# Optimization experiments

Hardware: AMD Instinct MI355X
Metric: run time of the kernel (lower is better)

## Reference

```python
import jax, jax.numpy as jnp
import numpy as np

B, N, C, H, R = 4, 1568, 768, 12, 256
D = C // H
MLP_H = 4 * C
EPS = 1e-5  # torch LayerNorm default


def _ln(x, g, b):
    mu = jnp.mean(x, -1, keepdims=True)
    var = jnp.var(x, -1, keepdims=True)
    return (x - mu) / jnp.sqrt(var + EPS) * g + b


def setup_inputs() -> dict:
    key = jax.random.key(0)
    ks = jax.random.split(key, 6)
    s = 0.02
    return {
        "x": jax.random.normal(ks[0], (B, N, C), jnp.float32),
        "size": jnp.ones((B, N, 1), jnp.float32),  # ToMe token sizes
        "qkv_w": jax.random.normal(ks[1], (3 * C, C), jnp.float32) * s,
        "q_bias": jnp.zeros((C,), jnp.float32),
        "v_bias": jnp.zeros((C,), jnp.float32),
        "proj_w": jax.random.normal(ks[2], (C, C), jnp.float32) * s,
        "proj_b": jnp.zeros((C,), jnp.float32),
        "ln1_g": jnp.ones((C,), jnp.float32),
        "ln1_b": jnp.zeros((C,), jnp.float32),
        "ln2_g": jnp.ones((C,), jnp.float32),
        "ln2_b": jnp.zeros((C,), jnp.float32),
        "fc1_w": jax.random.normal(ks[3], (MLP_H, C), jnp.float32) * s,
        "fc1_b": jnp.zeros((MLP_H,), jnp.float32),
        "fc2_w": jax.random.normal(ks[4], (C, MLP_H), jnp.float32) * s,
        "fc2_b": jnp.zeros((C,), jnp.float32),
        "r": R,
    }


def reference(x, size, qkv_w, q_bias, v_bias, proj_w, proj_b,
              ln1_g, ln1_b, ln2_g, ln2_b, fc1_w, fc1_b, fc2_w, fc2_b, r):
    Bc, Nc, Cc = x.shape
    scale = D ** -0.5

    # ---- attention with log-size bias ----
    h = _ln(x, ln1_g, ln1_b)
    qkv_bias = jnp.concatenate([q_bias, jnp.zeros_like(v_bias), v_bias])
    qkv = h @ qkv_w.T + qkv_bias                      # [B,N,3C]
    qkv = qkv.reshape(Bc, Nc, 3, H, D).transpose(2, 0, 3, 1, 4)  # [3,B,H,N,D]
    q, k, v = qkv[0] * scale, qkv[1], qkv[2]
    attn = jnp.einsum('bhnd,bhmd->bhnm', q, k)
    attn = attn + jnp.log(size)[:, None, None, :, 0]  # per-key log-size bias
    attn = jax.nn.softmax(attn, axis=-1)
    o = jnp.einsum('bhnm,bhmd->bhnd', attn, v)
    o = o.transpose(0, 2, 1, 3).reshape(Bc, Nc, Cc)
    o = o @ proj_w.T + proj_b
    metric = k.mean(axis=1)                           # [B,N,D] mean over heads
    x = x + o

    # ---- bipartite soft matching (class_token=False, distill=False) ----
    m = metric / jnp.linalg.norm(metric, axis=-1, keepdims=True)
    a, bt = m[:, ::2], m[:, 1::2]                     # [B,Ta,D], [B,Tb,D]
    scores = jnp.einsum('bic,bjc->bij', a, bt)
    node_max = scores.max(axis=-1)                    # [B,Ta]
    node_idx = scores.argmax(axis=-1)                 # [B,Ta]
    edge_idx = jnp.argsort(-node_max, axis=-1)        # descending
    unm_idx = edge_idx[:, r:]                         # [B,Ta-r]
    src_idx = edge_idx[:, :r]                         # [B,r]
    dst_idx = jnp.take_along_axis(node_idx, src_idx, axis=-1)  # [B,r]

    def _merge_sum(t):  # t: [B,N,c]
        src, dst = t[:, ::2], t[:, 1::2]
        unm = jnp.take_along_axis(src, unm_idx[:, :, None], axis=1)
        sg = jnp.take_along_axis(src, src_idx[:, :, None], axis=1)
        dst = jax.vmap(lambda d, i, s: d.at[i].add(s))(dst, dst_idx, sg)
        return jnp.concatenate([unm, dst], axis=1)

    # merge_wavg: size-weighted average
    xm = _merge_sum(x * size)
    size_new = _merge_sum(size)
    x = xm / size_new                                 # [B,N-r,C]

    # ---- MLP ----
    h = _ln(x, ln2_g, ln2_b)
    h = jax.nn.gelu(h @ fc1_w.T + fc1_b, approximate=False)
    x = x + (h @ fc2_w.T + fc2_b)
    return x
```

## Files before the change

kernel.cpp:

```cpp
#include <hip/hip_runtime.h>
#include <stdint.h>

typedef unsigned short ushort_t;
typedef __attribute__((ext_vector_type(4))) float f32x4;
typedef __attribute__((ext_vector_type(8))) short bf16x8;

#define DEV __device__ __forceinline__

DEV ushort_t f2bf(float f) {
  uint32_t x = __float_as_uint(f);
  uint32_t r = (x + 0x7fffu + ((x >> 16) & 1u)) >> 16;
  return (ushort_t)r;
}

DEV f32x4 mfma16(bf16x8 a, bf16x8 b, f32x4 c) {
  return __builtin_amdgcn_mfma_f32_16x16x32_bf16(a, b, c, 0, 0, 0);
}

DEV bf16x8 ld_frag_lds(const ushort_t* p) {
  bf16x8 r;
  ((uint64_t*)&r)[0] = ((const uint64_t*)p)[0];
  ((uint64_t*)&r)[1] = ((const uint64_t*)p)[1];
  return r;
}
DEV bf16x8 ld_frag_g(const ushort_t* p) { return *(const bf16x8*)p; }

DEV float np_pw96(const float* a) {
  float r0 = a[0], r1 = a[1], r2 = a[2], r3 = a[3];
  float r4 = a[4], r5 = a[5], r6 = a[6], r7 = a[7];
  for (int i = 8; i < 96; i += 8) {
    r0 = __fadd_rn(r0, a[i]);     r1 = __fadd_rn(r1, a[i + 1]);
    r2 = __fadd_rn(r2, a[i + 2]); r3 = __fadd_rn(r3, a[i + 3]);
    r4 = __fadd_rn(r4, a[i + 4]); r5 = __fadd_rn(r5, a[i + 5]);
    r6 = __fadd_rn(r6, a[i + 6]); r7 = __fadd_rn(r7, a[i + 7]);
  }
  return __fadd_rn(__fadd_rn(__fadd_rn(r0, r1), __fadd_rn(r2, r3)),
                   __fadd_rn(__fadd_rn(r4, r5), __fadd_rn(r6, r7)));
}
DEV float np_pw768(const float* a) {
  float q0 = __fadd_rn(np_pw96(a +   0), np_pw96(a +  96));
  float q1 = __fadd_rn(np_pw96(a + 192), np_pw96(a + 288));
  float q2 = __fadd_rn(np_pw96(a + 384), np_pw96(a + 480));
  float q3 = __fadd_rn(np_pw96(a + 576), np_pw96(a + 672));
  return __fadd_rn(__fadd_rn(q0, q1), __fadd_rn(q2, q3));
}
DEV float np_pw64(const float* a) {
  float r0 = a[0], r1 = a[1], r2 = a[2], r3 = a[3];
  float r4 = a[4], r5 = a[5], r6 = a[6], r7 = a[7];
  for (int i = 8; i < 64; i += 8) {
    r0 = __fadd_rn(r0, a[i]);     r1 = __fadd_rn(r1, a[i + 1]);
    r2 = __fadd_rn(r2, a[i + 2]); r3 = __fadd_rn(r3, a[i + 3]);
    r4 = __fadd_rn(r4, a[i + 4]); r5 = __fadd_rn(r5, a[i + 5]);
    r6 = __fadd_rn(r6, a[i + 6]); r7 = __fadd_rn(r7, a[i + 7]);
  }
  return __fadd_rn(__fadd_rn(__fadd_rn(r0, r1), __fadd_rn(r2, r3)),
                   __fadd_rn(__fadd_rn(r4, r5), __fadd_rn(r6, r7)));
}

DEV float np_einsum_dot64(const float* __restrict__ a, const float* __restrict__ b) {
  float v0 = 0.f, v1 = 0.f, v2 = 0.f, v3 = 0.f;
#pragma unroll
  for (int B = 0; B < 4; B++) {
    const float* pa = a + B * 16;
    const float* pb = b + B * 16;
    float t;
    t  = __fadd_rn(__fmul_rn(pa[12], pb[12]), v0);
    t  = __fadd_rn(__fmul_rn(pa[8],  pb[8]),  t);
    t  = __fadd_rn(__fmul_rn(pa[4],  pb[4]),  t);
    v0 = __fadd_rn(__fmul_rn(pa[0],  pb[0]),  t);
    t  = __fadd_rn(__fmul_rn(pa[13], pb[13]), v1);
    t  = __fadd_rn(__fmul_rn(pa[9],  pb[9]),  t);
    t  = __fadd_rn(__fmul_rn(pa[5],  pb[5]),  t);
    v1 = __fadd_rn(__fmul_rn(pa[1],  pb[1]),  t);
    t  = __fadd_rn(__fmul_rn(pa[14], pb[14]), v2);
    t  = __fadd_rn(__fmul_rn(pa[10], pb[10]), t);
    t  = __fadd_rn(__fmul_rn(pa[6],  pb[6]),  t);
    v2 = __fadd_rn(__fmul_rn(pa[2],  pb[2]),  t);
    t  = __fadd_rn(__fmul_rn(pa[15], pb[15]), v3);
    t  = __fadd_rn(__fmul_rn(pa[11], pb[11]), t);
    t  = __fadd_rn(__fmul_rn(pa[7],  pb[7]),  t);
    v3 = __fadd_rn(__fmul_rn(pa[3],  pb[3]),  t);
  }
  return __fadd_rn(__fadd_rn(v0, v1), __fadd_rn(v2, v3));
}

DEV bool flt_lt(float a, float b) { return a < b || (b != b && a == a); }

__global__ void f32_to_bf16_k(const float* __restrict__ in, ushort_t* __restrict__ out, int n) {
  int i = blockIdx.x * 256 + threadIdx.x;
  if (i < n) out[i] = f2bf(in[i]);
}

__global__ __launch_bounds__(64) void lnm32_k(
    const float* __restrict__ x, const float* __restrict__ g, const float* __restrict__ bb,
    float* __restrict__ h32) {
  const int row = blockIdx.x, lane = threadIdx.x;
  __shared__ float xs[768];
  __shared__ float sq[768];
  __shared__ float stat[2];
  const float* xr = x + (size_t)row * 768;
  for (int c = lane; c < 768; c += 64) xs[c] = xr[c];
  __syncthreads();
  if (lane == 0) stat[0] = __fdiv_rn(np_pw768(xs), 768.0f);
  __syncthreads();
  const float mu = stat[0];
  for (int c = lane; c < 768; c += 64) {
    float d = __fsub_rn(xs[c], mu);
    sq[c] = __fmul_rn(d, d);
  }
  __syncthreads();
  if (lane == 0) {
    float var = __fdiv_rn(np_pw768(sq), 768.0f);
    stat[1] = __fsqrt_rn(__fadd_rn(var, 1e-5f));
  }
  __syncthreads();
  const float sf = stat[1];
  float* hr = h32 + (size_t)row * 768;
  for (int c = lane; c < 768; c += 64) {
    float t = __fsub_rn(xs[c], mu);
    t = __fdiv_rn(t, sf);
    t = __fmul_rn(t, g[c]);
    t = __fadd_rn(t, bb[c]);
    hr[c] = t;
  }
}

__global__ __launch_bounds__(128) void kmetric32_k(
    const float* __restrict__ h32, const float* __restrict__ qkv_w, float* __restrict__ k32) {
  __shared__ float hs[64][68];
  __shared__ float wsd[64][68];
  const int tid = threadIdx.x;
  const int tx = tid & 15, ty = tid >> 4;
  const int tok0 = blockIdx.x * 64, ch0 = blockIdx.y * 64;
  float acc[8][4];
  float part[8][4];
#pragma unroll
  for (int i = 0; i < 8; i++)
#pragma unroll
    for (int j = 0; j < 4; j++) { acc[i][j] = 0.f; part[i][j] = 0.f; }

  for (int chunk = 0; chunk < 12; chunk++) {
    const int c0 = chunk * 64;
    __syncthreads();
#pragma unroll
    for (int e = 0; e < 8; e++) {
      int flat = e * 128 + tid;
      int r = flat >> 4, c4 = (flat & 15) << 2;
      *(float4*)&hs[r][c4] = *(const float4*)&h32[(size_t)(tok0 + r) * 768 + c0 + c4];
    }
#pragma unroll
    for (int e = 0; e < 8; e++) {
      int flat = e * 128 + tid;
      int r = flat >> 4, c4 = (flat & 15) << 2;
      *(float4*)&wsd[r][c4] = *(const float4*)&qkv_w[(size_t)(768 + ch0 + r) * 768 + c0 + c4];
    }
    __syncthreads();
#pragma unroll 1
    for (int cq = 0; cq < 16; cq++) {
      float4 hv[8], wv[4];
#pragma unroll
      for (int i = 0; i < 8; i++) hv[i] = *(const float4*)&hs[ty + 8 * i][cq << 2];
#pragma unroll
      for (int j = 0; j < 4; j++) wv[j] = *(const float4*)&wsd[tx + 16 * j][cq << 2];
#pragma unroll
      for (int u = 0; u < 4; u++)
#pragma unroll
        for (int i = 0; i < 8; i++) {
          float hvu = ((const float*)&hv[i])[u];
#pragma unroll
          for (int j = 0; j < 4; j++)
            acc[i][j] = __fmaf_rn(hvu, ((const float*)&wv[j])[u], acc[i][j]);
        }
    }
    if (chunk == 4) {
#pragma unroll
      for (int i = 0; i < 8; i++)
#pragma unroll
        for (int j = 0; j < 4; j++) { part[i][j] = acc[i][j]; acc[i][j] = 0.f; }
    } else if (chunk == 9) {
#pragma unroll
      for (int i = 0; i < 8; i++)
#pragma unroll
        for (int j = 0; j < 4; j++) { part[i][j] = __fadd_rn(part[i][j], acc[i][j]); acc[i][j] = 0.f; }
    }
  }
#pragma unroll
  for (int i = 0; i < 8; i++)
#pragma unroll
    for (int j = 0; j < 4; j++) {
      size_t idx = (size_t)(tok0 + ty + 8 * i) * 768 + ch0 + tx + 16 * j;
      k32[idx] = __fadd_rn(part[i][j], acc[i][j]);
    }
}

__global__ __launch_bounds__(64) void hmean32_k(
    const float* __restrict__ k32, float* __restrict__ m32) {
  const int row = blockIdx.x, lane = threadIdx.x;
  __shared__ float sm[64];
  const float* kr = k32 + (size_t)row * 768;
  float m = kr[lane];
  for (int hh = 1; hh < 12; hh++) m = __fadd_rn(m, kr[hh * 64 + lane]);
  m = __fdiv_rn(m, 12.0f);
  sm[lane] = __fmul_rn(m, m);
  __syncthreads();
  float nrm = __fsqrt_rn(np_pw64(sm));
  m32[(size_t)row * 64 + lane] = __fdiv_rn(m, nrm);
}

__global__ __launch_bounds__(64) void scores32_k(
    const float* __restrict__ m32, float* __restrict__ nmax, int* __restrict__ nidx) {
  const int b = blockIdx.y, i = blockIdx.x, lane = threadIdx.x;
  const float* mb = m32 + (size_t)b * 1568 * 64;
  __shared__ float av[64];
  __shared__ float bv[64];
  __shared__ int bj[64];
  av[lane] = mb[(size_t)(2 * i) * 64 + lane];
  __syncthreads();
  float best = -1e30f; int bidx = 0;
  for (int j = lane; j < 784; j += 64) {
    const float* br = mb + (size_t)(2 * j + 1) * 64;
    float dot = np_einsum_dot64(av, br);
    if (dot > best) { best = dot; bidx = j; }
  }
  bv[lane] = best; bj[lane] = bidx;
  __syncthreads();
  if (lane == 0) {
    float bb_ = bv[0]; int bi_ = bj[0];
    for (int l = 1; l < 64; l++)
      if (bv[l] > bb_ || (bv[l] == bb_ && bj[l] < bi_)) { bb_ = bv[l]; bi_ = bj[l]; }
    nmax[b * 784 + i] = bb_;
    nidx[b * 784 + i] = bi_;
  }
}

__global__ void zflag_k(int* tflag) { if (threadIdx.x == 0) tflag[0] = 0; }

__global__ __launch_bounds__(256) void rank_fast_k(
    const float* __restrict__ nmax, const int* __restrict__ nidx,
    int* __restrict__ eidx, int* __restrict__ didx, int* __restrict__ tflag) {
  const int b = blockIdx.x;
  __shared__ float sv[784];
  __shared__ int s_ei[784];
  for (int i = threadIdx.x; i < 784; i += 256) sv[i] = nmax[b * 784 + i];
  __syncthreads();
  for (int i = threadIdx.x; i < 784; i += 256) {
    float v = sv[i]; int rank = 0;
    for (int j = 0; j < 784; j++) {
      float u = sv[j];
      rank += (u > v || (u == v && j < i)) ? 1 : 0;
    }
    s_ei[rank] = i;
  }
  __syncthreads();
  for (int r = threadIdx.x; r < 783; r += 256)
    if (sv[s_ei[r]] == sv[s_ei[r + 1]]) atomicOr(tflag, 1);
  for (int i = threadIdx.x; i < 784; i += 256) eidx[b * 784 + i] = s_ei[i];
  for (int i = threadIdx.x; i < 256; i += 256) didx[b * 256 + i] = nidx[b * 784 + s_ei[i]];
}

__global__ __launch_bounds__(64) void argsort_serial_k(
    const float* __restrict__ nmax, const int* __restrict__ nidx,
    int* __restrict__ eidx, int* __restrict__ didx, const int* __restrict__ tflag) {
  if (tflag[0] == 0) return;
  const int b = blockIdx.x;
  __shared__ float sv[784];
  __shared__ int tos[784];
  for (int i = threadIdx.x; i < 784; i += 64) { sv[i] = -nmax[b * 784 + i]; tos[i] = i; }
  __syncthreads();
  if (threadIdx.x == 0) {
    const int num = 784;
    int stck[100]; int sptr = 0;
    int dpth[100]; int psd = 0;
    int cdepth; { int n = num, m = 0; while (n >>= 1) m++; cdepth = m * 2; }
    int pl = 0, pr = num - 1;
    for (;;) {
      if (cdepth < 0) {
        int n = pr - pl + 1;
        int* a = &tos[pl] - 1;
        for (int l = n >> 1; l > 0; --l) {
          int tmp = a[l];
          int i2 = l, j2 = l * 2;
          while (j2 <= n) {
            if (j2 < n && flt_lt(sv[a[j2]], sv[a[j2 + 1]])) j2++;
            if (flt_lt(sv[tmp], sv[a[j2]])) { a[i2] = a[j2]; i2 = j2; j2 += j2; }
            else break;
          }
          a[i2] = tmp;
        }
        for (int n2 = n; n2 > 1;) {
          int tmp = a[n2]; a[n2] = a[1]; n2--;
          int i2 = 1, j2 = 2;
          while (j2 <= n2) {
            if (j2 < n2 && flt_lt(sv[a[j2]], sv[a[j2 + 1]])) j2++;
            if (flt_lt(sv[tmp], sv[a[j2]])) { a[i2] = a[j2]; i2 = j2; j2 += j2; }
            else break;
          }
          a[i2] = tmp;
        }
        goto stack_pop;
      }
      while ((pr - pl) > 15) {
        int t_;
        int pm = pl + ((pr - pl) >> 1);
        if (flt_lt(sv[tos[pm]], sv[tos[pl]])) { t_ = tos[pm]; tos[pm] = tos[pl]; tos[pl] = t_; }
        if (flt_lt(sv[tos[pr]], sv[tos[pm]])) { t_ = tos[pr]; tos[pr] = tos[pm]; tos[pm] = t_; }
        if (flt_lt(sv[tos[pm]], sv[tos[pl]])) { t_ = tos[pm]; tos[pm] = tos[pl]; tos[pl] = t_; }
        float vp = sv[tos[pm]];
        int pi = pl, pj = pr - 1;
        t_ = tos[pm]; tos[pm] = tos[pj]; tos[pj] = t_;
        for (;;) {
          do { ++pi; } while (flt_lt(sv[tos[pi]], vp));
          do { --pj; } while (flt_lt(vp, sv[tos[pj]]));
          if (pi >= pj) break;
          t_ = tos[pi]; tos[pi] = tos[pj]; tos[pj] = t_;
        }
        int pk = pr - 1;
        t_ = tos[pi]; tos[pi] = tos[pk]; tos[pk] = t_;
        if (pi - pl < pr - pi) { stck[sptr++] = pi + 1; stck[sptr++] = pr; pr = pi - 1; }
        else                   { stck[sptr++] = pl; stck[sptr++] = pi - 1; pl = pi + 1; }
        dpth[psd++] = --cdepth;
      }
      for (int pi2 = pl + 1; pi2 <= pr; pi2++) {
        int vi = tos[pi2]; float vp2 = sv[vi];
        int pj2 = pi2, pk2 = pi2 - 1;
        while (pj2 > pl && flt_lt(vp2, sv[tos[pk2]])) { tos[pj2--] = tos[pk2--]; }
        tos[pj2] = vi;
      }
stack_pop:
      if (sptr == 0) break;
      pr = stck[--sptr]; pl = stck[--sptr];
      cdepth = dpth[--psd];
    }
  }
  __syncthreads();
  for (int i = threadIdx.x; i < 784; i += 64) eidx[b * 784 + i] = tos[i];
  for (int i = threadIdx.x; i < 256; i += 64) didx[b * 256 + i] = nidx[b * 784 + tos[i]];
}

__global__ __launch_bounds__(256) void ln_k(
    const float* __restrict__ x, const float* __restrict__ g, const float* __restrict__ bb,
    ushort_t* __restrict__ hout, const float* __restrict__ size, float* __restrict__ ls) {
  const int row = blockIdx.x;
  const float* xr = x + (size_t)row * 768;
  const int t = threadIdx.x;
  float v0 = xr[t], v1 = xr[t + 256], v2 = xr[t + 512];
  float s = v0 + v1 + v2;
  float ss = v0 * v0 + v1 * v1 + v2 * v2;
#pragma unroll
  for (int w = 32; w >= 1; w >>= 1) { s += __shfl_down(s, w); ss += __shfl_down(ss, w); }
  __shared__ float red[8];
  const int wv = t >> 6;
  if ((t & 63) == 0) { red[wv] = s; red[4 + wv] = ss; }
  __syncthreads();
  s  = red[0] + red[1] + red[2] + red[3];
  ss = red[4] + red[5] + red[6] + red[7];
  const float mu = s * (1.f / 768.f);
  const float rstd = rsqrtf(ss * (1.f / 768.f) - mu * mu + 1e-5f);
  ushort_t* hr = hout + (size_t)row * 768;
  hr[t]       = f2bf((v0 - mu) * rstd * g[t]       + bb[t]);
  hr[t + 256] = f2bf((v1 - mu) * rstd * g[t + 256] + bb[t + 256]);
  hr[t + 512] = f2bf((v2 - mu) * rstd * g[t + 512] + bb[t + 512]);
  if (ls != nullptr && t == 0) ls[row] = logf(size[row]);
}

template <int EPI>
__global__ __launch_bounds__(256) void gemm_bt(
    const ushort_t* __restrict__ A, const ushort_t* __restrict__ W, int K,
    const float* __restrict__ bias0, const float* __restrict__ bias1,
    const float* __restrict__ res,
    ushort_t* __restrict__ ob0, ushort_t* __restrict__ ob1, ushort_t* __restrict__ ob2,
    float* __restrict__ of) {
  __shared__ ushort_t As[128][36];
  __shared__ ushort_t Bs[128][36];
  const int tid = threadIdx.x;
  const int lane = tid & 63, wave = tid >> 6;
  const int wm = (wave >> 1) * 64, wn = (wave & 1) * 64;
  const int fr = lane & 15, kb = (lane >> 4) * 8;
  const int bm = blockIdx.x * 128, bn = blockIdx.y * 128;
  f32x4 acc[4][4] = {};
  for (int k0 = 0; k0 < K; k0 += 32) {
    __syncthreads();
    for (int ch = tid; ch < 512; ch += 256) {
      int r = ch >> 2, cb = (ch & 3) * 8;
      uint4 va = *(const uint4*)(A + (size_t)(bm + r) * K + k0 + cb);
      *(uint2*)&As[r][cb]     = make_uint2(va.x, va.y);
      *(uint2*)&As[r][cb + 4] = make_uint2(va.z, va.w);
      uint4 vb = *(const uint4*)(W + (size_t)(bn + r) * K + k0 + cb);
      *(uint2*)&Bs[r][cb]     = make_uint2(vb.x, vb.y);
      *(uint2*)&Bs[r][cb + 4] = make_uint2(vb.z, vb.w);
    }
    __syncthreads();
    bf16x8 af[4], bfr[4];
#pragma unroll
    for (int i = 0; i < 4; i++) af[i]  = ld_frag_lds(&As[wm + i * 16 + fr][kb]);
#pragma unroll
    for (int i = 0; i < 4; i++) bfr[i] = ld_frag_lds(&Bs[wn + i * 16 + fr][kb]);
#pragma unroll
    for (int mi = 0; mi < 4; mi++)
#pragma unroll
      for (int ni = 0; ni < 4; ni++)
        acc[mi][ni] = mfma16(af[mi], bfr[ni], acc[mi][ni]);
  }
#pragma unroll
  for (int mi = 0; mi < 4; mi++)
#pragma unroll
    for (int ni = 0; ni < 4; ni++)
#pragma unroll
      for (int e = 0; e < 4; e++) {
        int m = bm + wm + mi * 16 + (lane >> 4) * 4 + e;
        int j = bn + wn + ni * 16 + fr;
        float val = acc[mi][ni][e];
        if constexpr (EPI == 0) {
          int which = j / 768;
          int loc = j - which * 768;
          int hh = loc >> 6, d = loc & 63;
          unsigned um = (unsigned)m;
          unsigned b = um / 1568u;
          unsigned n = um - b * 1568u;
          if (which == 0) {
            val = (val + bias0[loc]) * 0.125f;
            ob0[(((size_t)b * 12 + hh) * 1568 + n) * 64 + d] = f2bf(val);
          } else if (which == 1) {
            ob1[(((size_t)b * 12 + hh) * 1568 + n) * 64 + d] = f2bf(val);
          } else {
            val += bias1[loc];
            ob2[(((size_t)b * 12 + hh) * 64 + d) * 1568 + n] = f2bf(val);
          }
        } else if constexpr (EPI == 1) {
          size_t idx = (size_t)m * 768 + j;
          of[idx] = val + bias0[j] + res[idx];
        } else if constexpr (EPI == 2) {
          float v = val + bias0[j];
          v = 0.5f * v * (1.0f + erff(v * 0.70710678118654752f));
          ob0[(size_t)m * 3072 + j] = f2bf(v);
        } else {
          size_t idx = (size_t)m * 768 + j;
          of[idx] = val + bias0[j] + of[idx];
        }
      }
}

__global__ __launch_bounds__(448) void attn_k(
    const ushort_t* __restrict__ q, const ushort_t* __restrict__ k,
    const ushort_t* __restrict__ vt, const float* __restrict__ ls,
    ushort_t* __restrict__ o) {
  const int h = blockIdx.y, b = blockIdx.z;
  const int tid = threadIdx.x, wave = tid >> 6, lane = tid & 63;
  const int fr = lane & 15, hi = lane >> 4, kb = hi * 8;
  const ushort_t* qb  = q  + (size_t)(b * 12 + h) * 1568 * 64;
  const ushort_t* kbp = k  + (size_t)(b * 12 + h) * 1568 * 64;
  const ushort_t* vtb = vt + (size_t)(b * 12 + h) * 64 * 1568;
  const float* lsb = ls + b * 1568;
  const int q0 = (blockIdx.x * 7 + wave) * 16;
  __shared__ ushort_t Ks[2][32][68];
  __shared__ ushort_t Vs[2][64][36];
  __shared__ ushort_t Pls[7][16][36];
  bf16x8 aq0 = ld_frag_g(qb + (size_t)(q0 + fr) * 64 + kb);
  bf16x8 aq1 = ld_frag_g(qb + (size_t)(q0 + fr) * 64 + 32 + kb);
  float m_r = -1e30f, l_r = 0.f;
  f32x4 oacc[4] = {};
  const bool doK = (tid < 256);
  const int krow = tid >> 3, kcol = (tid & 7) * 8;
  const int vtid = tid - 192;
  const bool doV = (vtid >= 0);
  const int vrow = vtid >> 2, vcol = (vtid & 3) * 8;
  if (doK) {
    uint4 kv = *(const uint4*)(kbp + (size_t)krow * 64 + kcol);
    *(uint2*)&Ks[0][krow][kcol]     = make_uint2(kv.x, kv.y);
    *(uint2*)&Ks[0][krow][kcol + 4] = make_uint2(kv.z, kv.w);
  }
  if (doV) {
    uint4 vv = *(const uint4*)(vtb + (size_t)vrow * 1568 + vcol);
    *(uint2*)&Vs[0][vrow][vcol]     = make_uint2(vv.x, vv.y);
    *(uint2*)&Vs[0][vrow][vcol + 4] = make_uint2(vv.z, vv.w);
  }
  __syncthreads();
  for (int kt = 0; kt < 49; kt++) {
    const int key0 = kt * 32;
    const int cur = kt & 1;
    uint4 kvn, vvn;
    if (kt < 48) {
      if (doK) kvn = *(const uint4*)(kbp + (size_t)(key0 + 32 + krow) * 64 + kcol);
      if (doV) vvn = *(const uint4*)(vtb + (size_t)vrow * 1568 + key0 + 32 + vcol);
    }
    bf16x8 c0a = ld_frag_lds(&Ks[cur][fr][kb]);
    bf16x8 c0b = ld_frag_lds(&Ks[cur][fr][32 + kb]);
    bf16x8 c1a = ld_frag_lds(&Ks[cur][16 + fr][kb]);
    bf16x8 c1b = ld_frag_lds(&Ks[cur][16 + fr][32 + kb]);
    f32x4 sl = {0, 0, 0, 0}, sh = {0, 0, 0, 0};
    sl = mfma16(c0a, aq0, sl); sl = mfma16(c0b, aq1, sl);
    sh = mfma16(c1a, aq0, sh); sh = mfma16(c1b, aq1, sh);
    float4 lsl = *(const float4*)&lsb[key0 + hi * 4];
    float4 lsh = *(const float4*)&lsb[key0 + 16 + hi * 4];
    float v0 = sl[0] + lsl.x, v1 = sl[1] + lsl.y, v2 = sl[2] + lsl.z, v3 = sl[3] + lsl.w;
    float v4 = sh[0] + lsh.x, v5 = sh[1] + lsh.y, v6 = sh[2] + lsh.z, v7 = sh[3] + lsh.w;
    float mx = fmaxf(fmaxf(fmaxf(v0, v1), fmaxf(v2, v3)),
                     fmaxf(fmaxf(v4, v5), fmaxf(v6, v7)));
    mx = fmaxf(mx, __shfl_xor(mx, 16));
    mx = fmaxf(mx, __shfl_xor(mx, 32));
    if (!__all(mx <= m_r)) {
      float mnew = fmaxf(m_r, mx);
      float corr = __expf(m_r - mnew);
      m_r = mnew;
      l_r *= corr;
      float cb0 = __shfl(corr, hi * 4 + 0);
      float cb1 = __shfl(corr, hi * 4 + 1);
      float cb2 = __shfl(corr, hi * 4 + 2);
      float cb3 = __shfl(corr, hi * 4 + 3);
#pragma unroll
      for (int dt = 0; dt < 4; dt++) {
        oacc[dt][0] *= cb0; oacc[dt][1] *= cb1;
        oacc[dt][2] *= cb2; oacc[dt][3] *= cb3;
      }
    }
    float p0 = __expf(v0 - m_r), p1 = __expf(v1 - m_r);
    float p2 = __expf(v2 - m_r), p3 = __expf(v3 - m_r);
    float p4 = __expf(v4 - m_r), p5 = __expf(v5 - m_r);
    float p6 = __expf(v6 - m_r), p7 = __expf(v7 - m_r);
    float ps = ((p0 + p1) + (p2 + p3)) + ((p4 + p5) + (p6 + p7));
    ps += __shfl_xor(ps, 16);
    ps += __shfl_xor(ps, 32);
    l_r += ps;
    uint32_t w0 = (uint32_t)f2bf(p0) | ((uint32_t)f2bf(p1) << 16);
    uint32_t w1 = (uint32_t)f2bf(p2) | ((uint32_t)f2bf(p3) << 16);
    uint32_t w2 = (uint32_t)f2bf(p4) | ((uint32_t)f2bf(p5) << 16);
    uint32_t w3 = (uint32_t)f2bf(p6) | ((uint32_t)f2bf(p7) << 16);
    *(uint2*)&Pls[wave][fr][hi * 4]      = make_uint2(w0, w1);
    *(uint2*)&Pls[wave][fr][16 + hi * 4] = make_uint2(w2, w3);
    bf16x8 pa = ld_frag_lds(&Pls[wave][fr][kb]);
#pragma unroll
    for (int dt = 0; dt < 4; dt++) {
      bf16x8 bvv = ld_frag_lds(&Vs[cur][dt * 16 + fr][kb]);
      oacc[dt] = mfma16(pa, bvv, oacc[dt]);
    }
    if (kt < 48) {
      if (doK) {
        *(uint2*)&Ks[cur ^ 1][krow][kcol]     = make_uint2(kvn.x, kvn.y);
        *(uint2*)&Ks[cur ^ 1][krow][kcol + 4] = make_uint2(kvn.z, kvn.w);
      }
      if (doV) {
        *(uint2*)&Vs[cur ^ 1][vrow][vcol]     = make_uint2(vvn.x, vvn.y);
        *(uint2*)&Vs[cur ^ 1][vrow][vcol + 4] = make_uint2(vvn.z, vvn.w);
      }
    }
    __syncthreads();
  }
  float lb[4];
#pragma unroll
  for (int e = 0; e < 4; e++) lb[e] = __shfl(l_r, hi * 4 + e);
  const size_t obase = ((size_t)b * 1568 + q0) * 768 + h * 64;
#pragma unroll
  for (int dt = 0; dt < 4; dt++)
#pragma unroll
    for (int e = 0; e < 4; e++)
      o[obase + (size_t)(hi * 4 + e) * 768 + dt * 16 + fr] = f2bf(oacc[dt][e] / lb[e]);
}

__global__ __launch_bounds__(256) void merge_k(
    const float* __restrict__ xa, const float* __restrict__ size,
    const int* __restrict__ eidx, const int* __restrict__ didx,
    float* __restrict__ xm) {
  const int b = blockIdx.y, t = blockIdx.x;
  const float* xab = xa + (size_t)b * 1568 * 768;
  const float* szb = size + (size_t)b * 1568;
  const int* ei = eidx + b * 784;
  const int* di = didx + b * 256;
  float* outr = xm + ((size_t)b * 1312 + t) * 768;
  if (t < 528) {
    int tok = 2 * ei[256 + t];
    float s = szb[tok];
    const float* xr = xab + (size_t)tok * 768;
    for (int c = threadIdx.x; c < 768; c += 256) outr[c] = (xr[c] * s) / s;
  } else {
    int j = t - 528;
    int tok = 2 * j + 1;
    float sn = szb[tok];
    for (int s_ = 0; s_ < 256; s_++)
      if (di[s_] == j) sn += szb[2 * ei[s_]];
    for (int c = threadIdx.x; c < 768; c += 256) {
      float val = xab[(size_t)tok * 768 + c] * szb[tok];
      for (int s_ = 0; s_ < 256; s_++) {
        if (di[s_] == j) { int st = 2 * ei[s_]; val += xab[(size_t)st * 768 + c] * szb[st]; }
      }
      outr[c] = val / sn;
    }
  }
}

static const size_t OFF_QKVW  = 0;
static const size_t OFF_PROJW = OFF_QKVW  + 3538944;
static const size_t OFF_FC1W  = OFF_PROJW + 1179648;
static const size_t OFF_FC2W  = OFF_FC1W  + 4718592;
static const size_t OFF_LS    = OFF_FC2W  + 4718592;
static const size_t OFF_MET   = OFF_LS    + 25088;
static const size_t OFF_NMAX  = OFF_MET   + 1605632;
static const size_t OFF_NIDX  = OFF_NMAX  + 12544;
static const size_t OFF_EIDX  = OFF_NIDX  + 12544;
static const size_t OFF_DIDX  = OFF_EIDX  + 12544;
static const size_t OFF_TFLAG = OFF_DIDX  + 4096;
static const size_t OFF_H     = OFF_TFLAG + 256;
static const size_t OFF_BIG   = OFF_H     + 9633792;
static const size_t OFF_O     = OFF_BIG   + 32243712;
static const size_t OFF_XA    = OFF_O     + 9633792;
static const size_t WS_NEED   = OFF_XA    + 19267584;

extern "C" void kernel_launch(void* const* d_in, const int* in_sizes, int n_in,
                              void* d_out, int out_size, void* d_ws, size_t ws_size,
                              hipStream_t stream) {
  (void)in_sizes; (void)n_in; (void)out_size;
  if (ws_size < WS_NEED) return;

  const float* x      = (const float*)d_in[0];
  const float* size_p = (const float*)d_in[1];
  const float* qkv_w  = (const float*)d_in[2];
  const float* q_bias = (const float*)d_in[3];
  const float* v_bias = (const float*)d_in[4];
  const float* proj_w = (const float*)d_in[5];
  const float* proj_b = (const float*)d_in[6];
  const float* ln1_g  = (const float*)d_in[7];
  const float* ln1_b  = (const float*)d_in[8];
  const float* ln2_g  = (const float*)d_in[9];
  const float* ln2_b  = (const float*)d_in[10];
  const float* fc1_w  = (const float*)d_in[11];
  const float* fc1_b  = (const float*)d_in[12];
  const float* fc2_w  = (const float*)d_in[13];
  const float* fc2_b  = (const float*)d_in[14];

  char* ws = (char*)d_ws;
  ushort_t* qkvw_bf = (ushort_t*)(ws + OFF_QKVW);
  ushort_t* projw_bf= (ushort_t*)(ws + OFF_PROJW);
  ushort_t* fc1w_bf = (ushort_t*)(ws + OFF_FC1W);
  ushort_t* fc2w_bf = (ushort_t*)(ws + OFF_FC2W);
  float*    ls      = (float*)   (ws + OFF_LS);
  float*    m32     = (float*)   (ws + OFF_MET);
  float*    nmax    = (float*)   (ws + OFF_NMAX);
  int*      nidx    = (int*)     (ws + OFF_NIDX);
  int*      eidx    = (int*)     (ws + OFF_EIDX);
  int*      didx    = (int*)     (ws + OFF_DIDX);
  int*      tflag   = (int*)     (ws + OFF_TFLAG);
  ushort_t* h_bf    = (ushort_t*)(ws + OFF_H);
  ushort_t* q_bf    = (ushort_t*)(ws + OFF_BIG);
  ushort_t* k_bf    = (ushort_t*)(ws + OFF_BIG + 9633792);
  ushort_t* vt_bf   = (ushort_t*)(ws + OFF_BIG + 2 * 9633792);
  ushort_t* h3_bf   = (ushort_t*)(ws + OFF_BIG);
  float*    k32     = (float*)   (ws + OFF_BIG);
  ushort_t* o_bf    = (ushort_t*)(ws + OFF_O);
  float*    xa      = (float*)   (ws + OFF_XA);
  float*    h32     = (float*)   (ws + OFF_XA);
  float*    out     = (float*)d_out;

  f32_to_bf16_k<<<6912, 256, 0, stream>>>(qkv_w, qkvw_bf, 2304 * 768);
  f32_to_bf16_k<<<2304, 256, 0, stream>>>(proj_w, projw_bf, 768 * 768);
  f32_to_bf16_k<<<9216, 256, 0, stream>>>(fc1_w, fc1w_bf, 3072 * 768);
  f32_to_bf16_k<<<9216, 256, 0, stream>>>(fc2_w, fc2w_bf, 768 * 3072);

  zflag_k<<<1, 64, 0, stream>>>(tflag);
  lnm32_k<<<6272, 64, 0, stream>>>(x, ln1_g, ln1_b, h32);
  kmetric32_k<<<dim3(98, 12), 128, 0, stream>>>(h32, qkv_w, k32);
  hmean32_k<<<6272, 64, 0, stream>>>(k32, m32);
  scores32_k<<<dim3(784, 4), 64, 0, stream>>>(m32, nmax, nidx);
  rank_fast_k<<<4, 256, 0, stream>>>(nmax, nidx, eidx, didx, tflag);
  argsort_serial_k<<<4, 64, 0, stream>>>(nmax, nidx, eidx, didx, tflag);

  ln_k<<<6272, 256, 0, stream>>>(x, ln1_g, ln1_b, h_bf, size_p, ls);
  gemm_bt<0><<<dim3(49, 18), 256, 0, stream>>>(h_bf, qkvw_bf, 768, q_bias, v_bias,
                                               nullptr, q_bf, k_bf, vt_bf, nullptr);
  attn_k<<<dim3(14, 12, 4), 448, 0, stream>>>(q_bf, k_bf, vt_bf, ls, o_bf);
  gemm_bt<1><<<dim3(49, 6), 256, 0, stream>>>(o_bf, projw_bf, 768, proj_b, nullptr,
                                              x, nullptr, nullptr, nullptr, xa);

  merge_k<<<dim3(1312, 4), 256, 0, stream>>>(xa, size_p, eidx, didx, out);

  ln_k<<<5248, 256, 0, stream>>>(out, ln2_g, ln2_b, h_bf, nullptr, nullptr);
  gemm_bt<2><<<dim3(41, 24), 256, 0, stream>>>(h_bf, fc1w_bf, 768, fc1_b, nullptr,
                                               nullptr, h3_bf, nullptr, nullptr, nullptr);
  gemm_bt<3><<<dim3(41, 6), 256, 0, stream>>>(h3_bf, fc2w_bf, 3072, fc2_b, nullptr,
                                              nullptr, nullptr, nullptr, nullptr, out);
}
```

Measured before the change: 913.9 us.

## Load GEMM tiles directly to LDS and precompute merge source lists

The GEMM tile loads now use global_load_lds (direct global-to-LDS, 16 bytes per lane) instead of staging through registers, and the LDS tiles drop the row padding (stride 32 instead of 36). This removes VGPR round-trips and LDS store instructions on the load path, but the unpadded layout may raise LDS bank conflicts on fragment reads. Separately, the merge kernel has one thread build a shared list of the source tokens for each destination. All threads then loop only over that list instead of each thread scanning all 256 indices per column.

New measurement: 811.5 us. 1.13x faster.

```diff
diff --git a/kernel.cpp b/kernel.cpp
--- a/kernel.cpp
+++ b/kernel.cpp
@@ -24,6 +24,11 @@
   return r;
 }
 DEV bf16x8 ld_frag_g(const ushort_t* p) { return *(const bf16x8*)p; }
+
+DEV void gload_lds16(const ushort_t* g, ushort_t* l) {
+  __builtin_amdgcn_global_load_lds((const __attribute__((address_space(1))) void*)g,
+                                   (__attribute__((address_space(3))) void*)l, 16, 0, 0);
+}
 
 DEV float np_pw96(const float* a) {
   float r0 = a[0], r1 = a[1], r2 = a[2], r3 = a[3];
@@ -370,31 +375,32 @@
     const float* __restrict__ res,
     ushort_t* __restrict__ ob0, ushort_t* __restrict__ ob1, ushort_t* __restrict__ ob2,
     float* __restrict__ of) {
-  __shared__ ushort_t As[128][36];
-  __shared__ ushort_t Bs[128][36];
+  __shared__ ushort_t As[128 * 32];
+  __shared__ ushort_t Bs[128 * 32];
   const int tid = threadIdx.x;
   const int lane = tid & 63, wave = tid >> 6;
   const int wm = (wave >> 1) * 64, wn = (wave & 1) * 64;
   const int fr = lane & 15, kb = (lane >> 4) * 8;
   const int bm = blockIdx.x * 128, bn = blockIdx.y * 128;
+  const int rr = tid >> 2;
+  const int cb = (tid & 3) * 8;
+  ushort_t* ldA0 = As + wave * 512;
+  ushort_t* ldA1 = As + 2048 + wave * 512;
+  ushort_t* ldB0 = Bs + wave * 512;
+  ushort_t* ldB1 = Bs + 2048 + wave * 512;
   f32x4 acc[4][4] = {};
   for (int k0 = 0; k0 < K; k0 += 32) {
     __syncthreads();
-    for (int ch = tid; ch < 512; ch += 256) {
-      int r = ch >> 2, cb = (ch & 3) * 8;
-      uint4 va = *(const uint4*)(A + (size_t)(bm + r) * K + k0 + cb);
-      *(uint2*)&As[r][cb]     = make_uint2(va.x, va.y);
-      *(uint2*)&As[r][cb + 4] = make_uint2(va.z, va.w);
-      uint4 vb = *(const uint4*)(W + (size_t)(bn + r) * K + k0 + cb);
-      *(uint2*)&Bs[r][cb]     = make_uint2(vb.x, vb.y);
-      *(uint2*)&Bs[r][cb + 4] = make_uint2(vb.z, vb.w);
-    }
+    gload_lds16(A + (size_t)(bm + rr) * K + k0 + cb,      ldA0);
+    gload_lds16(A + (size_t)(bm + 64 + rr) * K + k0 + cb, ldA1);
+    gload_lds16(W + (size_t)(bn + rr) * K + k0 + cb,      ldB0);
+    gload_lds16(W + (size_t)(bn + 64 + rr) * K + k0 + cb, ldB1);
     __syncthreads();
     bf16x8 af[4], bfr[4];
 #pragma unroll
-    for (int i = 0; i < 4; i++) af[i]  = ld_frag_lds(&As[wm + i * 16 + fr][kb]);
-#pragma unroll
-    for (int i = 0; i < 4; i++) bfr[i] = ld_frag_lds(&Bs[wn + i * 16 + fr][kb]);
+    for (int i = 0; i < 4; i++) af[i]  = ld_frag_lds(&As[(wm + i * 16 + fr) * 32 + kb]);
+#pragma unroll
+    for (int i = 0; i < 4; i++) bfr[i] = ld_frag_lds(&Bs[(wn + i * 16 + fr) * 32 + kb]);
 #pragma unroll
     for (int mi = 0; mi < 4; mi++)
 #pragma unroll
@@ -574,13 +580,24 @@
   } else {
     int j = t - 528;
     int tok = 2 * j + 1;
-    float sn = szb[tok];
-    for (int s_ = 0; s_ < 256; s_++)
-      if (di[s_] == j) sn += szb[2 * ei[s_]];
+    __shared__ int lst[256];
+    __shared__ int s_cnt;
+    __shared__ float s_sn;
+    if (threadIdx.x == 0) {
+      int cnt = 0;
+      float sn = szb[tok];
+      for (int s_ = 0; s_ < 256; s_++)
+        if (di[s_] == j) { int st = 2 * ei[s_]; lst[cnt++] = st; sn += szb[st]; }
+      s_cnt = cnt; s_sn = sn;
+    }
+    __syncthreads();
+    const int n = s_cnt;
+    const float sn = s_sn;
     for (int c = threadIdx.x; c < 768; c += 256) {
       float val = xab[(size_t)tok * 768 + c] * szb[tok];
-      for (int s_ = 0; s_ < 256; s_++) {
-        if (di[s_] == j) { int st = 2 * ei[s_]; val += xab[(size_t)st * 768 + c] * szb[st]; }
+      for (int l = 0; l < n; l++) {
+        int st = lst[l];
+        val += xab[(size_t)st * 768 + c] * szb[st];
       }
       outr[c] = val / sn;
     }
```
